# Kernel optimization log

Hardware: AMD Instinct MI355X
Metric: run time of the kernel (lower is better)

The kernel has to match this reference:

```python
import jax, jax.numpy as jnp
import numpy as np

LOG100 = float(np.log(100.0))
EPS = 1e-12  # F.normalize eps


def _l2norm(x):
    # torch.nn.functional.normalize(x, dim=-1): x / max(||x||_2, eps)
    n = jnp.sqrt(jnp.sum(x * x, axis=-1, keepdims=True))
    return x / jnp.maximum(n, EPS)


def setup_inputs() -> dict:
    key = jax.random.key(0)
    k1, k2, k3, k4, k5 = jax.random.split(key, 5)
    B_, nH, N, d = 256, 8, 256, 64
    q = jax.random.normal(k1, (B_, nH, N, d), dtype=jnp.float32)
    k = jax.random.normal(k2, (B_, nH, N, d), dtype=jnp.float32)
    v = jax.random.normal(k3, (B_, nH, N, d), dtype=jnp.float32)
    logit_scale = jax.random.normal(k4, (nH, 1, 1), dtype=jnp.float32)
    bias = jax.random.normal(k5, (nH, N, N), dtype=jnp.float32)
    return {"q": q, "k": k, "v": v, "logit_scale": logit_scale, "bias": bias}


def reference(q, k, v, logit_scale, bias):
    B_, nH, N, d = q.shape
    # cosine-similarity attention (euclidean_dist=False branch)
    scores = jnp.einsum("bhnd,bhmd->bhnm", _l2norm(q), _l2norm(k))
    # attn_transform: Swin-v2-style clamped learned logit scale + rel-pos bias
    scale = jnp.exp(jnp.minimum(logit_scale, LOG100))  # (nH,1,1)
    scores = scores * scale[None] + bias[None]
    attn = jax.nn.softmax(scores, axis=-1)
    # attn_drop with p=0 is identity
    x = jnp.einsum("bhnm,bhmd->bhnd", attn, v)
    # reshape=True branch: x.transpose(1,2).reshape(B_, -1, H*head_dim) with H==N
    x = jnp.transpose(x, (0, 2, 1, 3)).reshape(B_, -1, N * d)  # (B_, nH, N*d)
    return x
```

## Files before the change

kernel.cpp:

```cpp
#include <hip/hip_runtime.h>

#define LOG100 4.605170185988091f
#define LOG2E  1.4426950408889634f

typedef _Float16 half8 __attribute__((ext_vector_type(8)));
typedef float f32x4 __attribute__((ext_vector_type(4)));

__global__ __launch_bounds__(256) void bias_pack(const float* __restrict__ bias,
                                                 unsigned* __restrict__ biasP) {
  __shared__ float tile[32][33];
  const int head = blockIdx.z;
  const int m0 = blockIdx.x * 32;
  const int n0 = blockIdx.y * 32;
  const float* src = bias + head * 65536;
  unsigned* dst = biasP + head * 32768;
  const int tx = threadIdx.x, ty = threadIdx.y;
#pragma unroll
  for (int i = ty; i < 32; i += 8) tile[i][tx] = src[(n0 + i) * 256 + m0 + tx];
  __syncthreads();
#pragma unroll
  for (int j = ty; j < 16; j += 8) {
    const float lo = tile[tx][2 * j] * LOG2E;
    const float hi = tile[tx][2 * j + 1] * LOG2E;
    dst[(m0 / 2 + j) * 256 + n0 + tx] =
        __builtin_bit_cast(unsigned, __builtin_amdgcn_cvt_pkrtz(lo, hi));
  }
}

template <bool USE_BT>
__global__ __launch_bounds__(1024, 8) void attn_kernel(
    const float* __restrict__ q, const float* __restrict__ k, const float* __restrict__ v,
    const float* __restrict__ logit_scale, const float* __restrict__ bias,
    const unsigned* __restrict__ biasP, float* __restrict__ out) {
  __shared__ __align__(16) char smem[65536];
  char* KnB = smem;
  char* VtB = smem + 32768;

  const int tid = threadIdx.x;
  const int wv = tid >> 6;
  const int lane = tid & 63;
  const int q16 = lane & 15;
  const int g = lane >> 4;
  const int head = blockIdx.x;
  const int b = blockIdx.y;

  const long base = ((long)(b * 8 + head)) * (256 * 64);
  const float* qp = q + base;
  const float* kp = k + base;
  const float* vp = v + base;

  const float scale2 = __expf(fminf(logit_scale[head], LOG100)) * LOG2E;
  const int qglob = wv * 16 + q16;

  half8 qfrag[2];
  {
    float qf[2][8];
    float ssq = 0.f;
#pragma unroll
    for (int dk = 0; dk < 2; ++dk) {
      const float4 x0 = *(const float4*)(qp + qglob * 64 + dk * 32 + g * 8);
      const float4 x1 = *(const float4*)(qp + qglob * 64 + dk * 32 + g * 8 + 4);
      qf[dk][0] = x0.x; qf[dk][1] = x0.y; qf[dk][2] = x0.z; qf[dk][3] = x0.w;
      qf[dk][4] = x1.x; qf[dk][5] = x1.y; qf[dk][6] = x1.z; qf[dk][7] = x1.w;
      ssq += x0.x * x0.x + x0.y * x0.y + x0.z * x0.z + x0.w * x0.w;
      ssq += x1.x * x1.x + x1.y * x1.y + x1.z * x1.z + x1.w * x1.w;
    }
    ssq += __shfl_xor(ssq, 16);
    ssq += __shfl_xor(ssq, 32);
    const float qinv = rsqrtf(fmaxf(ssq, 1e-24f));
#pragma unroll
    for (int dk = 0; dk < 2; ++dk)
#pragma unroll
      for (int j = 0; j < 8; ++j) qfrag[dk][j] = (_Float16)(qf[dk][j] * qinv);
  }

  {
    const int row_in = tid >> 4;
    const int seg = tid & 15;
#pragma unroll
    for (int it = 0; it < 4; ++it) {
      const int row = it * 64 + row_in;
      const float4 a = *(const float4*)(kp + row * 64 + seg * 4);
      float ss = a.x * a.x + a.y * a.y + a.z * a.z + a.w * a.w;
      ss += __shfl_xor(ss, 1);
      ss += __shfl_xor(ss, 2);
      ss += __shfl_xor(ss, 4);
      ss += __shfl_xor(ss, 8);
      const float inv = rsqrtf(fmaxf(ss, 1e-24f));
      union { _Float16 hh[4]; uint2 u; } pk4;
      pk4.hh[0] = (_Float16)(a.x * inv);
      pk4.hh[1] = (_Float16)(a.y * inv);
      pk4.hh[2] = (_Float16)(a.z * inv);
      pk4.hh[3] = (_Float16)(a.w * inv);
      *(uint2*)(KnB + row * 128 + ((seg * 8) ^ ((row & 7) << 4))) = pk4.u;
    }
  }

  {
    const int r = g;
    const int sx = q16;
#pragma unroll
    for (int it = 0; it < 4; ++it) {
      const int kv0 = (wv * 4 + it) * 4;
      float4 a = *(const float4*)(vp + (kv0 + r) * 64 + sx * 4);
      float e1 = (r & 1) ? a.x : a.y;
      float g1 = __shfl_xor(e1, 16);
      float e2 = (r & 1) ? a.z : a.w;
      float g2 = __shfl_xor(e2, 16);
      if (r & 1) { a.x = g1; a.z = g2; } else { a.y = g1; a.w = g2; }
      float e3 = (r & 2) ? a.x : a.z;
      float g3 = __shfl_xor(e3, 32);
      float e4 = (r & 2) ? a.y : a.w;
      float g4 = __shfl_xor(e4, 32);
      if (r & 2) { a.x = g3; a.y = g4; } else { a.z = g3; a.w = g4; }
      const int d = 4 * sx + r;
      const int col0 = (kv0 & ~31) + (((kv0 >> 2) & 3) << 3) + (((kv0 >> 4) & 1) << 2);
      union { _Float16 hh[4]; uint2 u; } pk4;
      pk4.hh[0] = (_Float16)a.x;
      pk4.hh[1] = (_Float16)a.y;
      pk4.hh[2] = (_Float16)a.z;
      pk4.hh[3] = (_Float16)a.w;
      *(uint2*)(VtB + d * 512 + ((col0 * 2) ^ ((d & 31) << 4))) = pk4.u;
    }
  }

  __syncthreads();

  f32x4 o[4] = {};
  float m = -1.0e30f, lsum = 0.f;

  const unsigned* bP = USE_BT ? (biasP + head * 32768 + qglob) : nullptr;
  const float* bF = USE_BT ? nullptr : (bias + head * 65536 + qglob * 256);

  for (int c = 0; c < 8; ++c) {
    unsigned bw[4];
    float bvf[8];
    if (USE_BT) {
#pragma unroll
      for (int kvt = 0; kvt < 2; ++kvt)
#pragma unroll
        for (int p = 0; p < 2; ++p) bw[kvt * 2 + p] = bP[(c * 16 + kvt * 8 + g * 2 + p) * 256];
    } else {
#pragma unroll
      for (int i = 0; i < 8; ++i)
        bvf[i] = bF[c * 32 + (i >> 2) * 16 + g * 4 + (i & 3)] * LOG2E;
    }

    const int rk0 = c * 32 + q16;
    const char* kb0 = KnB + rk0 * 128;
    const char* kb1 = KnB + (rk0 + 16) * 128;
    const int sw = (rk0 & 7) << 4;
    f32x4 s0 = {}, s1 = {};
#pragma unroll
    for (int dk = 0; dk < 2; ++dk) {
      const half8 kf0 = *(const half8*)(kb0 + ((g * 16 + dk * 64) ^ sw));
      s0 = __builtin_amdgcn_mfma_f32_16x16x32_f16(kf0, qfrag[dk], s0, 0, 0, 0);
      const half8 kf1 = *(const half8*)(kb1 + ((g * 16 + dk * 64) ^ sw));
      s1 = __builtin_amdgcn_mfma_f32_16x16x32_f16(kf1, qfrag[dk], s1, 0, 0, 0);
    }

    float sv[8];
    if (USE_BT) {
#pragma unroll
      for (int kvt = 0; kvt < 2; ++kvt)
#pragma unroll
        for (int p = 0; p < 2; ++p) {
          const _Float16* hp = (const _Float16*)&bw[kvt * 2 + p];
          const int i = kvt * 4 + 2 * p;
          const float* sp = (kvt == 0) ? (const float*)&s0 : (const float*)&s1;
          sv[i] = fmaf(sp[2 * p], scale2, (float)hp[0]);
          sv[i + 1] = fmaf(sp[2 * p + 1], scale2, (float)hp[1]);
        }
    } else {
#pragma unroll
      for (int i = 0; i < 4; ++i) sv[i] = fmaf(s0[i], scale2, bvf[i]);
#pragma unroll
      for (int i = 0; i < 4; ++i) sv[4 + i] = fmaf(s1[i], scale2, bvf[4 + i]);
    }

    float m4[4];
#pragma unroll
    for (int i = 0; i < 4; ++i) m4[i] = fmaxf(sv[2 * i], sv[2 * i + 1]);
    float mx = fmaxf(fmaxf(m4[0], m4[1]), fmaxf(m4[2], m4[3]));
    mx = fmaxf(mx, __shfl_xor(mx, 16));
    mx = fmaxf(mx, __shfl_xor(mx, 32));

    if (__any(mx > m + 8.0f)) {
      const float mnew = fmaxf(m, mx);
      const float corr = exp2f(m - mnew);
      lsum *= corr;
#pragma unroll
      for (int dt = 0; dt < 4; ++dt)
#pragma unroll
        for (int i = 0; i < 4; ++i) o[dt][i] *= corr;
      m = mnew;
    }

#pragma unroll
    for (int i = 0; i < 8; ++i) sv[i] = exp2f(sv[i] - m);
    float a4[4];
#pragma unroll
    for (int i = 0; i < 4; ++i) a4[i] = sv[2 * i] + sv[2 * i + 1];
    float psum = (a4[0] + a4[1]) + (a4[2] + a4[3]);
    psum += __shfl_xor(psum, 16);
    psum += __shfl_xor(psum, 32);
    lsum += psum;

    union { unsigned u[4]; half8 hh; } pf;
    pf.u[0] = __builtin_bit_cast(unsigned, __builtin_amdgcn_cvt_pkrtz(sv[0], sv[1]));
    pf.u[1] = __builtin_bit_cast(unsigned, __builtin_amdgcn_cvt_pkrtz(sv[2], sv[3]));
    pf.u[2] = __builtin_bit_cast(unsigned, __builtin_amdgcn_cvt_pkrtz(sv[4], sv[5]));
    pf.u[3] = __builtin_bit_cast(unsigned, __builtin_amdgcn_cvt_pkrtz(sv[6], sv[7]));

#pragma unroll
    for (int dt = 0; dt < 4; ++dt) {
      const int d = dt * 16 + q16;
      const char* vb = VtB + d * 512;
      const half8 vf = *(const half8*)(vb + ((c * 64 + g * 16) ^ ((d & 31) << 4)));
      o[dt] = __builtin_amdgcn_mfma_f32_16x16x32_f16(vf, pf.hh, o[dt], 0, 0, 0);
    }
  }

  __syncthreads();

  char* ob = smem + wv * 2048;
  const float invl = 1.0f / lsum;
#pragma unroll
  for (int dt = 0; dt < 4; ++dt) {
    uint2 w;
    w.x = __builtin_bit_cast(unsigned,
        __builtin_amdgcn_cvt_pkrtz(o[dt][0] * invl, o[dt][1] * invl));
    w.y = __builtin_bit_cast(unsigned,
        __builtin_amdgcn_cvt_pkrtz(o[dt][2] * invl, o[dt][3] * invl));
    *(uint2*)(ob + q16 * 128 + ((dt * 32 + g * 8) ^ (q16 << 3))) = w;
  }
  __asm__ __volatile__("s_waitcnt lgkmcnt(0)" ::: "memory");
  __builtin_amdgcn_sched_barrier(0);
  const int qr = lane >> 2;
  const int fc = lane & 3;
#pragma unroll
  for (int it = 0; it < 4; ++it) {
    const int s4 = fc + it * 4;
    union { uint2 u; _Float16 hh[4]; } rd4;
    rd4.u = *(const uint2*)(ob + qr * 128 + ((s4 * 8) ^ (qr << 3)));
    float4 val;
    val.x = (float)rd4.hh[0];
    val.y = (float)rd4.hh[1];
    val.z = (float)rd4.hh[2];
    val.w = (float)rd4.hh[3];
    *(float4*)(out + (((long)(b * 256 + wv * 16 + qr) * 8 + head) * 64 + s4 * 4)) = val;
  }
}

extern "C" void kernel_launch(void* const* d_in, const int* in_sizes, int n_in,
                              void* d_out, int out_size, void* d_ws, size_t ws_size,
                              hipStream_t stream) {
  (void)in_sizes; (void)n_in; (void)out_size;
  const float* q = (const float*)d_in[0];
  const float* k = (const float*)d_in[1];
  const float* v = (const float*)d_in[2];
  const float* ls = (const float*)d_in[3];
  const float* bias = (const float*)d_in[4];
  float* out = (float*)d_out;
  const size_t bpBytes = (size_t)8 * 128 * 256 * 4;
  if (ws_size >= bpBytes) {
    unsigned* biasP = (unsigned*)d_ws;
    bias_pack<<<dim3(8, 8, 8), dim3(32, 8), 0, stream>>>(bias, biasP);
    attn_kernel<true><<<dim3(8, 256), dim3(1024), 0, stream>>>(q, k, v, ls, bias, biasP, out);
  } else {
    attn_kernel<false><<<dim3(8, 256), dim3(1024), 0, stream>>>(q, k, v, ls, bias, nullptr, out);
  }
}
```

Baseline: 150.9 us.

## Make attention blocks persistent over 8 batches with register-prefetched K/V

Each block now loops over 8 batch items for a single head, with a grid of 256 blocks instead of 2048. While the current item is computed, it prefetches the next item's K and V into registers. The softmax max/sum cross-lane reductions are deferred: the max shuffle happens only when a rescale is needed, and the sum is reduced once at the end. The aim is to hide global load latency and cut launch and tail overhead. The cost is fewer blocks (256 on a 256-CU device, one block per CU), extra register pressure from the prefetch buffers (launch bounds relaxed to 4), and extra syncthreads per iteration.

```diff
diff --git a/kernel.cpp b/kernel.cpp
--- a/kernel.cpp
+++ b/kernel.cpp
@@ -28,7 +28,7 @@
 }
 
 template <bool USE_BT>
-__global__ __launch_bounds__(1024, 8) void attn_kernel(
+__global__ __launch_bounds__(1024, 4) void attn_kernel(
     const float* __restrict__ q, const float* __restrict__ k, const float* __restrict__ v,
     const float* __restrict__ logit_scale, const float* __restrict__ bias,
     const unsigned* __restrict__ biasP, float* __restrict__ out) {
@@ -40,47 +40,49 @@
   const int wv = tid >> 6;
   const int lane = tid & 63;
   const int q16 = lane & 15;
-  const int g = lane >> 4;
-  const int head = blockIdx.x;
-  const int b = blockIdx.y;
-
-  const long base = ((long)(b * 8 + head)) * (256 * 64);
-  const float* qp = q + base;
-  const float* kp = k + base;
-  const float* vp = v + base;
+  const int g4 = lane >> 4;
+  const int gb = blockIdx.x;
+  const int head = gb & 7;
+  const int bgrp = gb >> 3;
 
   const float scale2 = __expf(fminf(logit_scale[head], LOG100)) * LOG2E;
   const int qglob = wv * 16 + q16;
 
-  half8 qfrag[2];
+  const unsigned* bP = USE_BT ? (biasP + head * 32768 + qglob) : nullptr;
+  const float* bF = USE_BT ? nullptr : (bias + head * 65536 + qglob * 256);
+
+  const int krow_in = tid >> 4;
+  const int kseg = tid & 15;
+
+  float4 kReg[4], vReg[4];
   {
-    float qf[2][8];
-    float ssq = 0.f;
+    const long base0 = ((long)((bgrp * 8) * 8 + head)) * (256 * 64);
+    const float* kp = k + base0;
+    const float* vp = v + base0;
+#pragma unroll
+    for (int it = 0; it < 4; ++it) {
+      kReg[it] = *(const float4*)(kp + (it * 64 + krow_in) * 64 + kseg * 4);
+      vReg[it] = *(const float4*)(vp + ((wv * 4 + it) * 4 + g4) * 64 + q16 * 4);
+    }
+  }
+
+#pragma unroll 1
+  for (int t = 0; t < 8; ++t) {
+    const int b = bgrp * 8 + t;
+    const long base = ((long)(b * 8 + head)) * (256 * 64);
+    const float* qp = q + base;
+
+    float4 qraw[4];
 #pragma unroll
     for (int dk = 0; dk < 2; ++dk) {
-      const float4 x0 = *(const float4*)(qp + qglob * 64 + dk * 32 + g * 8);
-      const float4 x1 = *(const float4*)(qp + qglob * 64 + dk * 32 + g * 8 + 4);
-      qf[dk][0] = x0.x; qf[dk][1] = x0.y; qf[dk][2] = x0.z; qf[dk][3] = x0.w;
-      qf[dk][4] = x1.x; qf[dk][5] = x1.y; qf[dk][6] = x1.z; qf[dk][7] = x1.w;
-      ssq += x0.x * x0.x + x0.y * x0.y + x0.z * x0.z + x0.w * x0.w;
-      ssq += x1.x * x1.x + x1.y * x1.y + x1.z * x1.z + x1.w * x1.w;
-    }
-    ssq += __shfl_xor(ssq, 16);
-    ssq += __shfl_xor(ssq, 32);
-    const float qinv = rsqrtf(fmaxf(ssq, 1e-24f));
-#pragma unroll
-    for (int dk = 0; dk < 2; ++dk)
-#pragma unroll
-      for (int j = 0; j < 8; ++j) qfrag[dk][j] = (_Float16)(qf[dk][j] * qinv);
-  }
-
-  {
-    const int row_in = tid >> 4;
-    const int seg = tid & 15;
+      qraw[2 * dk] = *(const float4*)(qp + qglob * 64 + dk * 32 + g4 * 8);
+      qraw[2 * dk + 1] = *(const float4*)(qp + qglob * 64 + dk * 32 + g4 * 8 + 4);
+    }
+
 #pragma unroll
     for (int it = 0; it < 4; ++it) {
-      const int row = it * 64 + row_in;
-      const float4 a = *(const float4*)(kp + row * 64 + seg * 4);
+      const int row = it * 64 + krow_in;
+      const float4 a = kReg[it];
       float ss = a.x * a.x + a.y * a.y + a.z * a.z + a.w * a.w;
       ss += __shfl_xor(ss, 1);
       ss += __shfl_xor(ss, 2);
@@ -92,17 +94,14 @@
       pk4.hh[1] = (_Float16)(a.y * inv);
       pk4.hh[2] = (_Float16)(a.z * inv);
       pk4.hh[3] = (_Float16)(a.w * inv);
-      *(uint2*)(KnB + row * 128 + ((seg * 8) ^ ((row & 7) << 4))) = pk4.u;
-    }
-  }
-
-  {
-    const int r = g;
-    const int sx = q16;
+      *(uint2*)(KnB + row * 128 + ((kseg * 8) ^ ((row & 7) << 4))) = pk4.u;
+    }
+
 #pragma unroll
     for (int it = 0; it < 4; ++it) {
       const int kv0 = (wv * 4 + it) * 4;
-      float4 a = *(const float4*)(vp + (kv0 + r) * 64 + sx * 4);
+      float4 a = vReg[it];
+      const int r = g4;
       float e1 = (r & 1) ? a.x : a.y;
       float g1 = __shfl_xor(e1, 16);
       float e2 = (r & 1) ? a.z : a.w;
@@ -111,9 +110,9 @@
       float e3 = (r & 2) ? a.x : a.z;
       float g3 = __shfl_xor(e3, 32);
       float e4 = (r & 2) ? a.y : a.w;
-      float g4 = __shfl_xor(e4, 32);
-      if (r & 2) { a.x = g3; a.y = g4; } else { a.z = g3; a.w = g4; }
-      const int d = 4 * sx + r;
+      float g4v = __shfl_xor(e4, 32);
+      if (r & 2) { a.x = g3; a.y = g4v; } else { a.z = g3; a.w = g4v; }
+      const int d = 4 * q16 + r;
       const int col0 = (kv0 & ~31) + (((kv0 >> 2) & 3) << 3) + (((kv0 >> 4) & 1) << 2);
       union { _Float16 hh[4]; uint2 u; } pk4;
       pk4.hh[0] = (_Float16)a.x;
@@ -122,133 +121,187 @@
       pk4.hh[3] = (_Float16)a.w;
       *(uint2*)(VtB + d * 512 + ((col0 * 2) ^ ((d & 31) << 4))) = pk4.u;
     }
-  }
-
-  __syncthreads();
-
-  f32x4 o[4] = {};
-  float m = -1.0e30f, lsum = 0.f;
-
-  const unsigned* bP = USE_BT ? (biasP + head * 32768 + qglob) : nullptr;
-  const float* bF = USE_BT ? nullptr : (bias + head * 65536 + qglob * 256);
-
-  for (int c = 0; c < 8; ++c) {
-    unsigned bw[4];
-    float bvf[8];
-    if (USE_BT) {
-#pragma unroll
-      for (int kvt = 0; kvt < 2; ++kvt)
-#pragma unroll
-        for (int p = 0; p < 2; ++p) bw[kvt * 2 + p] = bP[(c * 16 + kvt * 8 + g * 2 + p) * 256];
-    } else {
-#pragma unroll
-      for (int i = 0; i < 8; ++i)
-        bvf[i] = bF[c * 32 + (i >> 2) * 16 + g * 4 + (i & 3)] * LOG2E;
-    }
-
-    const int rk0 = c * 32 + q16;
-    const char* kb0 = KnB + rk0 * 128;
-    const char* kb1 = KnB + (rk0 + 16) * 128;
-    const int sw = (rk0 & 7) << 4;
-    f32x4 s0 = {}, s1 = {};
-#pragma unroll
-    for (int dk = 0; dk < 2; ++dk) {
-      const half8 kf0 = *(const half8*)(kb0 + ((g * 16 + dk * 64) ^ sw));
-      s0 = __builtin_amdgcn_mfma_f32_16x16x32_f16(kf0, qfrag[dk], s0, 0, 0, 0);
-      const half8 kf1 = *(const half8*)(kb1 + ((g * 16 + dk * 64) ^ sw));
-      s1 = __builtin_amdgcn_mfma_f32_16x16x32_f16(kf1, qfrag[dk], s1, 0, 0, 0);
-    }
-
-    float sv[8];
-    if (USE_BT) {
-#pragma unroll
-      for (int kvt = 0; kvt < 2; ++kvt)
-#pragma unroll
-        for (int p = 0; p < 2; ++p) {
-          const _Float16* hp = (const _Float16*)&bw[kvt * 2 + p];
-          const int i = kvt * 4 + 2 * p;
-          const float* sp = (kvt == 0) ? (const float*)&s0 : (const float*)&s1;
-          sv[i] = fmaf(sp[2 * p], scale2, (float)hp[0]);
-          sv[i + 1] = fmaf(sp[2 * p + 1], scale2, (float)hp[1]);
+
+    half8 qfrag[2];
+    {
+      float ssq = 0.f;
+#pragma unroll
+      for (int i = 0; i < 4; ++i) {
+        const float4 x = qraw[i];
+        ssq += x.x * x.x + x.y * x.y + x.z * x.z + x.w * x.w;
+      }
+      ssq += __shfl_xor(ssq, 16);
+      ssq += __shfl_xor(ssq, 32);
+      const float qinv = rsqrtf(fmaxf(ssq, 1e-24f));
+#pragma unroll
+      for (int dk = 0; dk < 2; ++dk) {
+        const float4 x0 = qraw[2 * dk];
+        const float4 x1 = qraw[2 * dk + 1];
+        qfrag[dk][0] = (_Float16)(x0.x * qinv);
+        qfrag[dk][1] = (_Float16)(x0.y * qinv);
+        qfrag[dk][2] = (_Float16)(x0.z * qinv);
+        qfrag[dk][3] = (_Float16)(x0.w * qinv);
+        qfrag[dk][4] = (_Float16)(x1.x * qinv);
+        qfrag[dk][5] = (_Float16)(x1.y * qinv);
+        qfrag[dk][6] = (_Float16)(x1.z * qinv);
+        qfrag[dk][7] = (_Float16)(x1.w * qinv);
+      }
+    }
+
+    {
+      const int bn = bgrp * 8 + (t < 7 ? t + 1 : 7);
+      const long baseN = ((long)(bn * 8 + head)) * (256 * 64);
+      const float* kpN = k + baseN;
+      const float* vpN = v + baseN;
+#pragma unroll
+      for (int it = 0; it < 4; ++it) {
+        kReg[it] = *(const float4*)(kpN + (it * 64 + krow_in) * 64 + kseg * 4);
+        vReg[it] = *(const float4*)(vpN + ((wv * 4 + it) * 4 + g4) * 64 + q16 * 4);
+      }
+    }
+
+    __syncthreads();
+
+    f32x4 o0 = {}, o1 = {}, o2 = {}, o3 = {};
+    float m = -1.0e30f, lsum = 0.f;
+
+    for (int c = 0; c < 8; ++c) {
+      unsigned bw[4];
+      float bvf[8];
+      if (USE_BT) {
+#pragma unroll
+        for (int kvt = 0; kvt < 2; ++kvt)
+#pragma unroll
+          for (int p = 0; p < 2; ++p) bw[kvt * 2 + p] = bP[(c * 16 + kvt * 8 + g4 * 2 + p) * 256];
+      } else {
+#pragma unroll
+        for (int i = 0; i < 8; ++i)
+          bvf[i] = bF[c * 32 + (i >> 2) * 16 + g4 * 4 + (i & 3)] * LOG2E;
+      }
+
+      const int rk0 = c * 32 + q16;
+      const char* kb0 = KnB + rk0 * 128;
+      const char* kb1 = KnB + (rk0 + 16) * 128;
+      const int sw = (rk0 & 7) << 4;
+      f32x4 s0 = {}, s1 = {};
+#pragma unroll
+      for (int dk = 0; dk < 2; ++dk) {
+        const half8 kf0 = *(const half8*)(kb0 + ((g4 * 16 + dk * 64) ^ sw));
+        s0 = __builtin_amdgcn_mfma_f32_16x16x32_f16(kf0, qfrag[dk], s0, 0, 0, 0);
+        const half8 kf1 = *(const half8*)(kb1 + ((g4 * 16 + dk * 64) ^ sw));
+        s1 = __builtin_amdgcn_mfma_f32_16x16x32_f16(kf1, qfrag[dk], s1, 0, 0, 0);
+      }
+
+      float sv[8];
+      if (USE_BT) {
+#pragma unroll
+        for (int kvt = 0; kvt < 2; ++kvt)
+#pragma unroll
+          for (int p = 0; p < 2; ++p) {
+            const _Float16* hp = (const _Float16*)&bw[kvt * 2 + p];
+            const int i = kvt * 4 + 2 * p;
+            const float* sp = (kvt == 0) ? (const float*)&s0 : (const float*)&s1;
+            sv[i] = fmaf(sp[2 * p], scale2, (float)hp[0]);
+            sv[i + 1] = fmaf(sp[2 * p + 1], scale2, (float)hp[1]);
+          }
+      } else {
+#pragma unroll
+        for (int i = 0; i < 4; ++i) sv[i] = fmaf(s0[i], scale2, bvf[i]);
+#pragma unroll
+        for (int i = 0; i < 4; ++i) sv[4 + i] = fmaf(s1[i], scale2, bvf[4 + i]);
+      }
+
+      float m4[4];
+#pragma unroll
+      for (int i = 0; i < 4; ++i) m4[i] = fmaxf(sv[2 * i], sv[2 * i + 1]);
+      const float mxl = fmaxf(fmaxf(m4[0], m4[1]), fmaxf(m4[2], m4[3]));
+      if (__any(mxl > m + 8.0f)) {
+        float mx = fmaxf(mxl, __shfl_xor(mxl, 16));
+        mx = fmaxf(mx, __shfl_xor(mx, 32));
+        const float mnew = fmaxf(m, mx);
+        const float corr = exp2f(m - mnew);
+        lsum *= corr;
+#pragma unroll
+        for (int i = 0; i < 4; ++i) {
+          o0[i] *= corr; o1[i] *= corr; o2[i] *= corr; o3[i] *= corr;
         }
-    } else {
-#pragma unroll
-      for (int i = 0; i < 4; ++i) sv[i] = fmaf(s0[i], scale2, bvf[i]);
-#pragma unroll
-      for (int i = 0; i < 4; ++i) sv[4 + i] = fmaf(s1[i], scale2, bvf[4 + i]);
-    }
-
-    float m4[4];
-#pragma unroll
-    for (int i = 0; i < 4; ++i) m4[i] = fmaxf(sv[2 * i], sv[2 * i + 1]);
-    float mx = fmaxf(fmaxf(m4[0], m4[1]), fmaxf(m4[2], m4[3]));
-    mx = fmaxf(mx, __shfl_xor(mx, 16));
-    mx = fmaxf(mx, __shfl_xor(mx, 32));
-
-    if (__any(mx > m + 8.0f)) {
-      const float mnew = fmaxf(m, mx);
-      const float corr = exp2f(m - mnew);
-      lsum *= corr;
-#pragma unroll
-      for (int dt = 0; dt < 4; ++dt)
-#pragma unroll
-        for (int i = 0; i < 4; ++i) o[dt][i] *= corr;
-      m = mnew;
-    }
-
-#pragma unroll
-    for (int i = 0; i < 8; ++i) sv[i] = exp2f(sv[i] - m);
-    float a4[4];
-#pragma unroll
-    for (int i = 0; i < 4; ++i) a4[i] = sv[2 * i] + sv[2 * i + 1];
-    float psum = (a4[0] + a4[1]) + (a4[2] + a4[3]);
-    psum += __shfl_xor(psum, 16);
-    psum += __shfl_xor(psum, 32);
-    lsum += psum;
-
-    union { unsigned u[4]; half8 hh; } pf;
-    pf.u[0] = __builtin_bit_cast(unsigned, __builtin_amdgcn_cvt_pkrtz(sv[0], sv[1]));
-    pf.u[1] = __builtin_bit_cast(unsigned, __builtin_amdgcn_cvt_pkrtz(sv[2], sv[3]));
-    pf.u[2] = __builtin_bit_cast(unsigned, __builtin_amdgcn_cvt_pkrtz(sv[4], sv[5]));
-    pf.u[3] = __builtin_bit_cast(unsigned, __builtin_amdgcn_cvt_pkrtz(sv[6], sv[7]));
-
-#pragma unroll
-    for (int dt = 0; dt < 4; ++dt) {
-      const int d = dt * 16 + q16;
-      const char* vb = VtB + d * 512;
-      const half8 vf = *(const half8*)(vb + ((c * 64 + g * 16) ^ ((d & 31) << 4)));
-      o[dt] = __builtin_amdgcn_mfma_f32_16x16x32_f16(vf, pf.hh, o[dt], 0, 0, 0);
-    }
-  }
-
-  __syncthreads();
-
-  char* ob = smem + wv * 2048;
-  const float invl = 1.0f / lsum;
-#pragma unroll
-  for (int dt = 0; dt < 4; ++dt) {
-    uint2 w;
-    w.x = __builtin_bit_cast(unsigned,
-        __builtin_amdgcn_cvt_pkrtz(o[dt][0] * invl, o[dt][1] * invl));
-    w.y = __builtin_bit_cast(unsigned,
-        __builtin_amdgcn_cvt_pkrtz(o[dt][2] * invl, o[dt][3] * invl));
-    *(uint2*)(ob + q16 * 128 + ((dt * 32 + g * 8) ^ (q16 << 3))) = w;
-  }
-  __asm__ __volatile__("s_waitcnt lgkmcnt(0)" ::: "memory");
-  __builtin_amdgcn_sched_barrier(0);
-  const int qr = lane >> 2;
-  const int fc = lane & 3;
-#pragma unroll
-  for (int it = 0; it < 4; ++it) {
-    const int s4 = fc + it * 4;
-    union { uint2 u; _Float16 hh[4]; } rd4;
-    rd4.u = *(const uint2*)(ob + qr * 128 + ((s4 * 8) ^ (qr << 3)));
-    float4 val;
-    val.x = (float)rd4.hh[0];
-    val.y = (float)rd4.hh[1];
-    val.z = (float)rd4.hh[2];
-    val.w = (float)rd4.hh[3];
-    *(float4*)(out + (((long)(b * 256 + wv * 16 + qr) * 8 + head) * 64 + s4 * 4)) = val;
+        m = mnew;
+      }
+
+#pragma unroll
+      for (int i = 0; i < 8; ++i) sv[i] = exp2f(sv[i] - m);
+      float a4[4];
+#pragma unroll
+      for (int i = 0; i < 4; ++i) a4[i] = sv[2 * i] + sv[2 * i + 1];
+      lsum += (a4[0] + a4[1]) + (a4[2] + a4[3]);
+
+      union { unsigned u[4]; half8 hh; } pf;
+      pf.u[0] = __builtin_bit_cast(unsigned, __builtin_amdgcn_cvt_pkrtz(sv[0], sv[1]));
+      pf.u[1] = __builtin_bit_cast(unsigned, __builtin_amdgcn_cvt_pkrtz(sv[2], sv[3]));
+      pf.u[2] = __builtin_bit_cast(unsigned, __builtin_amdgcn_cvt_pkrtz(sv[4], sv[5]));
+      pf.u[3] = __builtin_bit_cast(unsigned, __builtin_amdgcn_cvt_pkrtz(sv[6], sv[7]));
+
+      {
+        const int d = 0 * 16 + q16;
+        const half8 vf = *(const half8*)(VtB + d * 512 + ((c * 64 + g4 * 16) ^ ((d & 31) << 4)));
+        o0 = __builtin_amdgcn_mfma_f32_16x16x32_f16(vf, pf.hh, o0, 0, 0, 0);
+      }
+      {
+        const int d = 1 * 16 + q16;
+        const half8 vf = *(const half8*)(VtB + d * 512 + ((c * 64 + g4 * 16) ^ ((d & 31) << 4)));
+        o1 = __builtin_amdgcn_mfma_f32_16x16x32_f16(vf, pf.hh, o1, 0, 0, 0);
+      }
+      {
+        const int d = 2 * 16 + q16;
+        const half8 vf = *(const half8*)(VtB + d * 512 + ((c * 64 + g4 * 16) ^ ((d & 31) << 4)));
+        o2 = __builtin_amdgcn_mfma_f32_16x16x32_f16(vf, pf.hh, o2, 0, 0, 0);
+      }
+      {
+        const int d = 3 * 16 + q16;
+        const half8 vf = *(const half8*)(VtB + d * 512 + ((c * 64 + g4 * 16) ^ ((d & 31) << 4)));
+        o3 = __builtin_amdgcn_mfma_f32_16x16x32_f16(vf, pf.hh, o3, 0, 0, 0);
+      }
+    }
+
+    __syncthreads();
+
+    lsum += __shfl_xor(lsum, 16);
+    lsum += __shfl_xor(lsum, 32);
+    char* ob = smem + wv * 2048;
+    const float invl = 1.0f / lsum;
+    {
+      uint2 w;
+      w.x = __builtin_bit_cast(unsigned, __builtin_amdgcn_cvt_pkrtz(o0[0] * invl, o0[1] * invl));
+      w.y = __builtin_bit_cast(unsigned, __builtin_amdgcn_cvt_pkrtz(o0[2] * invl, o0[3] * invl));
+      *(uint2*)(ob + q16 * 128 + ((0 * 32 + g4 * 8) ^ (q16 << 3))) = w;
+      w.x = __builtin_bit_cast(unsigned, __builtin_amdgcn_cvt_pkrtz(o1[0] * invl, o1[1] * invl));
+      w.y = __builtin_bit_cast(unsigned, __builtin_amdgcn_cvt_pkrtz(o1[2] * invl, o1[3] * invl));
+      *(uint2*)(ob + q16 * 128 + ((1 * 32 + g4 * 8) ^ (q16 << 3))) = w;
+      w.x = __builtin_bit_cast(unsigned, __builtin_amdgcn_cvt_pkrtz(o2[0] * invl, o2[1] * invl));
+      w.y = __builtin_bit_cast(unsigned, __builtin_amdgcn_cvt_pkrtz(o2[2] * invl, o2[3] * invl));
+      *(uint2*)(ob + q16 * 128 + ((2 * 32 + g4 * 8) ^ (q16 << 3))) = w;
+      w.x = __builtin_bit_cast(unsigned, __builtin_amdgcn_cvt_pkrtz(o3[0] * invl, o3[1] * invl));
+      w.y = __builtin_bit_cast(unsigned, __builtin_amdgcn_cvt_pkrtz(o3[2] * invl, o3[3] * invl));
+      *(uint2*)(ob + q16 * 128 + ((3 * 32 + g4 * 8) ^ (q16 << 3))) = w;
+    }
+    __asm__ __volatile__("s_waitcnt lgkmcnt(0)" ::: "memory");
+    __builtin_amdgcn_sched_barrier(0);
+    const int qr = lane >> 2;
+    const int fc = lane & 3;
+#pragma unroll
+    for (int it = 0; it < 4; ++it) {
+      const int s4 = fc + it * 4;
+      union { uint2 u; _Float16 hh[4]; } rd4;
+      rd4.u = *(const uint2*)(ob + qr * 128 + ((s4 * 8) ^ (qr << 3)));
+      float4 val;
+      val.x = (float)rd4.hh[0];
+      val.y = (float)rd4.hh[1];
+      val.z = (float)rd4.hh[2];
+      val.w = (float)rd4.hh[3];
+      *(float4*)(out + (((long)(b * 256 + wv * 16 + qr) * 8 + head) * 64 + s4 * 4)) = val;
+    }
+
+    __syncthreads();
   }
 }
 
@@ -266,8 +319,8 @@
   if (ws_size >= bpBytes) {
     unsigned* biasP = (unsigned*)d_ws;
     bias_pack<<<dim3(8, 8, 8), dim3(32, 8), 0, stream>>>(bias, biasP);
-    attn_kernel<true><<<dim3(8, 256), dim3(1024), 0, stream>>>(q, k, v, ls, bias, biasP, out);
+    attn_kernel<true><<<dim3(256), dim3(1024), 0, stream>>>(q, k, v, ls, bias, biasP, out);
   } else {
-    attn_kernel<false><<<dim3(8, 256), dim3(1024), 0, stream>>>(q, k, v, ls, bias, nullptr, out);
+    attn_kernel<false><<<dim3(256), dim3(1024), 0, stream>>>(q, k, v, ls, bias, nullptr, out);
   }
 }
```

Measured after the change: 328.5 us. +117.6%, slower.
